# Kernel tuning notes

Hardware: AMD Instinct MI355X
Metric: run time of the kernel (lower is better)

Reference implementation:

```python
import jax, jax.numpy as jnp
import numpy as np

B, T, C, H = 4, 2048, 1024, 16
DH = C // H


def setup_inputs() -> dict:
    key = jax.random.key(0)
    k1, k2, k3 = jax.random.split(key, 3)
    x = jax.random.normal(k1, (B, T, C), dtype=jnp.float32)
    w_attn = jax.random.normal(k2, (C, 3 * C), dtype=jnp.float32) * 0.02
    w_proj = jax.random.normal(k3, (C, C), dtype=jnp.float32) * 0.02
    return {"x": x, "w_attn": w_attn, "w_proj": w_proj}


def reference(x, w_attn, w_proj):
    b, t, c = x.shape
    qkv = x @ w_attn  # [B,T,3C]
    q, k, v = jnp.split(qkv, 3, axis=2)
    # [B,T,C] -> [B,H,T,DH]
    q = q.reshape(b, t, H, DH).transpose(0, 2, 1, 3)
    k = k.reshape(b, t, H, DH).transpose(0, 2, 1, 3)
    v = v.reshape(b, t, H, DH).transpose(0, 2, 1, 3)
    scale = 1.0 / np.sqrt(DH).astype(np.float32)
    att = jnp.einsum('bhqd,bhkd->bhqk', q, k) * scale  # [B,H,T,T]
    causal = jnp.tril(jnp.ones((t, t), dtype=bool))
    att = jnp.where(causal[None, None], att, jnp.finfo(att.dtype).min)
    att = jax.nn.softmax(att, axis=-1)
    y = jnp.einsum('bhqk,bhkd->bhqd', att, v)  # [B,H,T,DH]
    y = y.transpose(0, 2, 1, 3).reshape(b, t, c)
    return y @ w_proj
```

## Files before the change

### kernel.cpp

```cpp
#include <hip/hip_runtime.h>
#include <hip/hip_bf16.h>

typedef unsigned short u16;
typedef __attribute__((ext_vector_type(8))) __bf16 bf16x8;
typedef __attribute__((ext_vector_type(4))) float f32x4;
typedef __attribute__((ext_vector_type(16))) float f32x16;
typedef u16 u16x8 __attribute__((ext_vector_type(8)));
typedef u16x8 u16x8a __attribute__((may_alias));
typedef f32x4 f32x4a __attribute__((may_alias));

constexpr int Bz = 4, T = 2048, Cdim = 1024, H = 16, DH = 64;
constexpr int Mrows = Bz * T;
constexpr int N_QKV = 3 * Cdim;
constexpr int Kdim = Cdim;
constexpr float C1 = 0.18033688011118324f;
constexpr float C2 = 34.62468098133512f;

__device__ __forceinline__ u16 f2bf(float f) {
    union { float f; unsigned u; } x; x.f = f;
    if ((x.u & 0x7f800000u) == 0x7f800000u) return 0;
    unsigned r = x.u + 0x7fffu + ((x.u >> 16) & 1u);
    return (u16)(r >> 16);
}

__device__ __forceinline__ bf16x8 as_bf(u16x8 v) {
    union { u16x8 u; bf16x8 b; } x; x.u = v; return x.b;
}

__device__ __forceinline__ void gload_lds16(const u16* g, u16* l) {
    __builtin_amdgcn_global_load_lds(
        (const __attribute__((address_space(1))) void*)g,
        (__attribute__((address_space(3))) void*)l, 16, 0, 0);
}

__device__ __forceinline__ float exp2_raw(float x) {
    float r;
    asm("v_exp_f32 %0, %1" : "=v"(r) : "v"(x));
    return r;
}

__global__ __launch_bounds__(256) void prep_kernel(
    const float* __restrict__ X, u16* __restrict__ Xb, long n8,
    const float* __restrict__ W1, u16* __restrict__ WT1,
    const float* __restrict__ W2, u16* __restrict__ WT2)
{
    const int bid = blockIdx.x;
    if (bid < 2048) {
        for (long i = bid * 256 + threadIdx.x; i < n8; i += (long)2048 * 256) {
            f32x4 a0 = *(const f32x4a*)&X[i * 8];
            f32x4 a1 = *(const f32x4a*)&X[i * 8 + 4];
            u16x8 p;
            p[0] = f2bf(a0[0]); p[1] = f2bf(a0[1]); p[2] = f2bf(a0[2]); p[3] = f2bf(a0[3]);
            p[4] = f2bf(a1[0]); p[5] = f2bf(a1[1]); p[6] = f2bf(a1[2]); p[7] = f2bf(a1[3]);
            *(u16x8a*)&Xb[i * 8] = p;
        }
    } else if (bid < 3584) {
        const int tb = bid - 2048;
        const int n = (tb % (N_QKV / 256)) * 256 + threadIdx.x;
        const int k8 = (tb / (N_QKV / 256)) * 8;
        u16x8 p;
#pragma unroll
        for (int i = 0; i < 8; ++i) p[i] = f2bf(W1[(long)(k8 + i) * N_QKV + n]);
        *(u16x8a*)&WT1[(long)n * Kdim + k8] = p;
    } else {
        const int tb = bid - 3584;
        const int n = (tb % (Cdim / 256)) * 256 + threadIdx.x;
        const int k8 = (tb / (Cdim / 256)) * 8;
        u16x8 p;
#pragma unroll
        for (int i = 0; i < 8; ++i) p[i] = f2bf(W2[(long)(k8 + i) * Cdim + n]);
        *(u16x8a*)&WT2[(long)n * Kdim + k8] = p;
    }
}

__global__ __launch_bounds__(256) void transpose_cvt(
    const float* __restrict__ W, u16* __restrict__ WT, int K, int N)
{
    const int n = blockIdx.x * 256 + threadIdx.x;
    const int k8 = blockIdx.y * 8;
    u16x8 p;
#pragma unroll
    for (int i = 0; i < 8; ++i) p[i] = f2bf(W[(long)(k8 + i) * N + n]);
    *(u16x8a*)&WT[(long)n * K + k8] = p;
}

template <int MODE>
__global__ __launch_bounds__(256) void gemm_kernel(
    const u16* __restrict__ Ab, const u16* __restrict__ Bw,
    float* __restrict__ out,
    u16* __restrict__ qb, u16* __restrict__ kb, u16* __restrict__ vtb,
    int Nsz, int Ksz)
{
    constexpr int BM = 128, BN = 128, BK = 64;
    __shared__ __align__(16) u16 As[BM * BK];
    __shared__ __align__(16) u16 Bt[BN * BK];

    const int tid = threadIdx.x;
    const int w = tid >> 6, lane = tid & 63, quad = lane >> 4, lr = lane & 15;
    const int wr = (w >> 1) * 64, wc = (w & 1) * 64;
    const int m0 = blockIdx.y * BM, n0 = blockIdx.x * BN;
    const int lr7 = lr & 7;

    const int lrow = lane >> 3;
    const int lcol = ((lane & 7) ^ lrow) * 8;

    f32x4 acc[4][4] = {};

    for (int k0 = 0; k0 < Ksz; k0 += BK) {
#pragma unroll
        for (int s = 0; s < 4; ++s) {
            const int chunk = w * 4 + s;
            const int r = chunk * 8 + lrow;
            const u16* asrc;
            if (MODE == 1) {
                asrc = &Ab[(long)(m0 + r) * Ksz + k0 + lcol];
            } else {
                const int m = m0 + r, b = m >> 11, t = m & (T - 1), h = k0 >> 6;
                asrc = &Ab[(((long)(b * H + h)) * T + t) * DH + lcol];
            }
            gload_lds16(asrc, &As[chunk * 512]);
            gload_lds16(&Bw[(long)(n0 + r) * Ksz + k0 + lcol], &Bt[chunk * 512]);
        }
        __syncthreads();

#pragma unroll
        for (int ks = 0; ks < 2; ++ks) {
            bf16x8 af[4];
#pragma unroll
            for (int it = 0; it < 4; ++it)
                af[it] = as_bf(*(const u16x8a*)
                    &As[(wr + it * 16 + lr) * BK + (((ks * 4 + quad) ^ lr7) * 8)]);
#pragma unroll
            for (int jt = 0; jt < 4; ++jt) {
                bf16x8 bfv = as_bf(*(const u16x8a*)
                    &Bt[(wc + jt * 16 + lr) * BK + (((ks * 4 + quad) ^ lr7) * 8)]);
#pragma unroll
                for (int it = 0; it < 4; ++it)
                    acc[it][jt] = __builtin_amdgcn_mfma_f32_16x16x32_bf16(af[it], bfv, acc[it][jt], 0, 0, 0);
            }
        }
        __syncthreads();
    }

#pragma unroll
    for (int it = 0; it < 4; ++it) {
#pragma unroll
        for (int jt = 0; jt < 4; ++jt) {
#pragma unroll
            for (int r = 0; r < 4; ++r) {
                int m = m0 + wr + it * 16 + quad * 4 + r;
                int n = n0 + wc + jt * 16 + lr;
                if (MODE == 2) {
                    out[(long)m * Nsz + n] = acc[it][jt][r];
                } else {
                    u16 hv = f2bf(acc[it][jt][r]);
                    int b = m >> 11, t = m & (T - 1);
                    int sec = n >> 10, rem = n & 1023, h = rem >> 6, d = rem & 63;
                    int bh = b * H + h;
                    if (sec == 0)      qb [((long)bh * T + t) * DH + d] = hv;
                    else if (sec == 1) kb [((long)bh * T + t) * DH + d] = hv;
                    else               vtb[((long)bh * DH + d) * T + t] = hv;
                }
            }
        }
    }
}

__global__ __launch_bounds__(256) void attn_kernel(
    const u16* qbuf, const u16* __restrict__ kbuf,
    const u16* __restrict__ vtbuf, u16* yb)
{
    constexpr int KS = 72;
    __shared__ __align__(16) u16 Ks[2][64 * KS];
    __shared__ __align__(16) u16 Vts[2][64 * KS];

    const int tid = threadIdx.x;
    const int w = tid >> 6, lane = tid & 63;
    const int l31 = lane & 31, hi = lane >> 5, hi4 = hi * 4, hi8 = hi * 8;
    const int bh    = blockIdx.x;
    const int pairi = blockIdx.y;

    const u16* qbase  = qbuf  + (long)bh * T * DH;
    const u16* kbase  = kbuf  + (long)bh * T * DH;
    const u16* vtbase = vtbuf + (long)bh * DH * T;
    u16* ybase = yb + (long)bh * T * DH;

    const int sr0 = tid >> 3;
    const int sc0 = (tid & 7) * 8;

    u16x8 ones_u;
#pragma unroll
    for (int i = 0; i < 8; ++i) ones_u[i] = 0x3F80;
    const bf16x8 onesf = as_bf(ones_u);

    for (int qsel = 0; qsel < 2; ++qsel) {
        const int qblk = qsel ? (15 - pairi) : pairi;
        const int q0 = qblk * 128;

        bf16x8 qf[4];
#pragma unroll
        for (int dsl = 0; dsl < 4; ++dsl)
            qf[dsl] = as_bf(*(const u16x8a*)
                &qbase[(q0 + w * 32 + l31) * DH + dsl * 16 + hi8]);

        f32x16 o[2] = {};
        f32x16 accl = {};

        const int ktmax = 2 * qblk + 1;

        u16x8 kreg[2], vreg[2];
#pragma unroll
        for (int s = 0; s < 2; ++s) {
            int row = sr0 + s * 32;
            kreg[s] = *(const u16x8a*)&kbase[(long)row * DH + sc0];
            vreg[s] = *(const u16x8a*)&vtbase[(long)row * T + sc0];
        }

        for (int kt = 0; kt <= ktmax; ++kt) {
            const int buf = kt & 1;
#pragma unroll
            for (int s = 0; s < 2; ++s) {
                int row = sr0 + s * 32;
                *(u16x8a*)&Ks[buf][row * KS + sc0]  = kreg[s];
                *(u16x8a*)&Vts[buf][row * KS + sc0] = vreg[s];
            }
            __syncthreads();

            if (kt < ktmax) {
#pragma unroll
                for (int s = 0; s < 2; ++s) {
                    int row = sr0 + s * 32;
                    kreg[s] = *(const u16x8a*)&kbase[(long)((kt + 1) * 64 + row) * DH + sc0];
                    vreg[s] = *(const u16x8a*)&vtbase[(long)row * T + (kt + 1) * 64 + sc0];
                }
            }

            f32x16 sp[2] = {};
#pragma unroll
            for (int dsl = 0; dsl < 4; ++dsl) {
#pragma unroll
                for (int nt = 0; nt < 2; ++nt) {
                    bf16x8 kf = as_bf(*(const u16x8a*)
                        &Ks[buf][(nt * 32 + l31) * KS + dsl * 16 + hi8]);
                    sp[nt] = __builtin_amdgcn_mfma_f32_32x32x16_bf16(
                        kf, qf[dsl], sp[nt], 0, 0, 0);
                }
            }

            const bool need_mask = (kt >= 2 * qblk);
            const int qrow = q0 + w * 32 + l31;
#pragma unroll
            for (int nt = 0; nt < 2; ++nt) {
#pragma unroll
                for (int reg = 0; reg < 16; ++reg) {
                    float e = exp2_raw(__builtin_fmaf(sp[nt][reg], C1, -C2));
                    if (need_mask) {
                        int key = kt * 64 + nt * 32 + ((reg & 3) + 8 * (reg >> 2)) + hi4;
                        e = (key <= qrow) ? e : 0.f;
                    }
                    sp[nt][reg] = e;
                }
            }

            unsigned wv[2][8];
#pragma unroll
            for (int nt = 0; nt < 2; ++nt)
#pragma unroll
                for (int g = 0; g < 4; ++g)
#pragma unroll
                    for (int h = 0; h < 2; ++h)
                        asm("v_cvt_pk_bf16_f32 %0, %1, %2"
                            : "=v"(wv[nt][g * 2 + h])
                            : "v"(sp[nt][g * 4 + 2 * h]), "v"(sp[nt][g * 4 + 2 * h + 1]));

#pragma unroll
            for (int sl = 0; sl < 4; ++sl) {
                const int nt = sl >> 1, s2 = (sl & 1) * 2;
                unsigned a0 = wv[nt][s2 * 2 + 0], a1 = wv[nt][s2 * 2 + 1];
                unsigned a2 = wv[nt][(s2 + 1) * 2 + 0], a3 = wv[nt][(s2 + 1) * 2 + 1];
                asm("v_permlane32_swap_b32 %0, %1" : "+v"(a0), "+v"(a2));
                asm("v_permlane32_swap_b32 %0, %1" : "+v"(a1), "+v"(a3));
                union { unsigned u[4]; bf16x8 b; } pk;
                pk.u[0] = a0; pk.u[1] = a1; pk.u[2] = a2; pk.u[3] = a3;
                accl = __builtin_amdgcn_mfma_f32_32x32x16_bf16(
                    pk.b, onesf, accl, 0, 0, 0);
#pragma unroll
                for (int dt = 0; dt < 2; ++dt) {
                    bf16x8 vf = as_bf(*(const u16x8a*)
                        &Vts[buf][(dt * 32 + l31) * KS + sl * 16 + hi8]);
                    o[dt] = __builtin_amdgcn_mfma_f32_32x32x16_bf16(
                        pk.b, vf, o[dt], 0, 0, 0);
                }
            }
        }

#pragma unroll
        for (int reg = 0; reg < 16; ++reg) {
            float rl;
            asm("v_rcp_f32 %0, %1" : "=v"(rl) : "v"(accl[reg]));
            const int cr = (reg & 3) + 8 * (reg >> 2) + hi4;
            const int t = q0 + w * 32 + cr;
#pragma unroll
            for (int dt = 0; dt < 2; ++dt)
                ybase[(long)t * DH + dt * 32 + l31] = f2bf(o[dt][reg] * rl);
        }
    }
}

extern "C" void kernel_launch(void* const* d_in, const int* in_sizes, int n_in,
                              void* d_out, int out_size, void* d_ws, size_t ws_size,
                              hipStream_t stream) {
    const float* x      = (const float*)d_in[0];
    const float* w_attn = (const float*)d_in[1];
    const float* w_proj = (const float*)d_in[2];
    float* out = (float*)d_out;

    const size_t per = (size_t)Bz * H * T * DH;
    u16* qb  = (u16*)d_ws;
    u16* kb  = qb + per;
    u16* vtb = kb + per;

    u16* xb     = (u16*)d_out;
    u16* watT   = xb + (size_t)Mrows * Kdim;

    const bool big_ws = ws_size >= ((size_t)50 << 20);
    u16* wprojT = big_ws ? (u16*)((char*)d_ws + ((size_t)48 << 20)) : kb;

    dim3 blk(256);
    prep_kernel<<<dim3(big_ws ? 4096 : 3584), blk, 0, stream>>>(
        x, xb, (long)Mrows * Kdim / 8, w_attn, watT, w_proj, wprojT);
    gemm_kernel<1><<<dim3(N_QKV / 128, Mrows / 128), blk, 0, stream>>>(
        xb, watT, nullptr, qb, kb, vtb, N_QKV, Kdim);
    attn_kernel<<<dim3(64, 8), blk, 0, stream>>>(qb, kb, vtb, qb);
    if (!big_ws)
        transpose_cvt<<<dim3(Cdim / 256, Kdim / 8), blk, 0, stream>>>(
            w_proj, wprojT, Kdim, Cdim);
    gemm_kernel<2><<<dim3(Cdim / 128, Mrows / 128), blk, 0, stream>>>(
        qb, wprojT, out, nullptr, nullptr, nullptr, Cdim, Kdim);
}
```

Before: 263.2 us.

## Process both paired query blocks in one KV sweep to share K/V tile loads

Rather than looping over the two paired query blocks one after another, the kernel now keeps both query blocks' fragments and accumulators live and walks the key/value tiles once, up to the larger block's causal limit. Each staged K/V tile in shared memory is consumed by block B and, while still within its causal range, by block A. This removes the second pass of global loads, LDS stores and barriers for the shorter block. The cost is roughly double the accumulator and query registers, which may lower occupancy or cause spills.

```diff
diff --git a/kernel.cpp b/kernel.cpp
--- a/kernel.cpp
+++ b/kernel.cpp
@@ -193,116 +193,128 @@
     for (int i = 0; i < 8; ++i) ones_u[i] = 0x3F80;
     const bf16x8 onesf = as_bf(ones_u);
 
-    for (int qsel = 0; qsel < 2; ++qsel) {
-        const int qblk = qsel ? (15 - pairi) : pairi;
-        const int q0 = qblk * 128;
-
-        bf16x8 qf[4];
-#pragma unroll
-        for (int dsl = 0; dsl < 4; ++dsl)
-            qf[dsl] = as_bf(*(const u16x8a*)
-                &qbase[(q0 + w * 32 + l31) * DH + dsl * 16 + hi8]);
-
-        f32x16 o[2] = {};
-        f32x16 accl = {};
-
-        const int ktmax = 2 * qblk + 1;
-
-        u16x8 kreg[2], vreg[2];
+    const int qbA = pairi, qbB = 15 - pairi;
+    const int q0A = qbA * 128, q0B = qbB * 128;
+    const int ktmaxA = 2 * qbA + 1;
+    const int ktmaxB = 2 * qbB + 1;
+
+    bf16x8 qfA[4], qfB[4];
+#pragma unroll
+    for (int dsl = 0; dsl < 4; ++dsl) {
+        qfA[dsl] = as_bf(*(const u16x8a*)
+            &qbase[(q0A + w * 32 + l31) * DH + dsl * 16 + hi8]);
+        qfB[dsl] = as_bf(*(const u16x8a*)
+            &qbase[(q0B + w * 32 + l31) * DH + dsl * 16 + hi8]);
+    }
+
+    f32x16 oA[2] = {}, oB[2] = {};
+    f32x16 acclA = {}, acclB = {};
+
+    auto compute = [&](const bf16x8* qf, f32x16* o, f32x16& accl,
+                       int q0, int qblk, int kt, int buf) {
+        f32x16 sp[2] = {};
+#pragma unroll
+        for (int dsl = 0; dsl < 4; ++dsl) {
+#pragma unroll
+            for (int nt = 0; nt < 2; ++nt) {
+                bf16x8 kf = as_bf(*(const u16x8a*)
+                    &Ks[buf][(nt * 32 + l31) * KS + dsl * 16 + hi8]);
+                sp[nt] = __builtin_amdgcn_mfma_f32_32x32x16_bf16(
+                    kf, qf[dsl], sp[nt], 0, 0, 0);
+            }
+        }
+
+        const bool need_mask = (kt >= 2 * qblk);
+        const int qrow = q0 + w * 32 + l31;
+#pragma unroll
+        for (int nt = 0; nt < 2; ++nt) {
+#pragma unroll
+            for (int reg = 0; reg < 16; ++reg) {
+                float e = exp2_raw(__builtin_fmaf(sp[nt][reg], C1, -C2));
+                if (need_mask) {
+                    int key = kt * 64 + nt * 32 + ((reg & 3) + 8 * (reg >> 2)) + hi4;
+                    e = (key <= qrow) ? e : 0.f;
+                }
+                sp[nt][reg] = e;
+            }
+        }
+
+        unsigned wv[2][8];
+#pragma unroll
+        for (int nt = 0; nt < 2; ++nt)
+#pragma unroll
+            for (int g = 0; g < 4; ++g)
+#pragma unroll
+                for (int h = 0; h < 2; ++h)
+                    asm("v_cvt_pk_bf16_f32 %0, %1, %2"
+                        : "=v"(wv[nt][g * 2 + h])
+                        : "v"(sp[nt][g * 4 + 2 * h]), "v"(sp[nt][g * 4 + 2 * h + 1]));
+
+#pragma unroll
+        for (int sl = 0; sl < 4; ++sl) {
+            const int nt = sl >> 1, s2 = (sl & 1) * 2;
+            unsigned a0 = wv[nt][s2 * 2 + 0], a1 = wv[nt][s2 * 2 + 1];
+            unsigned a2 = wv[nt][(s2 + 1) * 2 + 0], a3 = wv[nt][(s2 + 1) * 2 + 1];
+            asm("v_permlane32_swap_b32 %0, %1" : "+v"(a0), "+v"(a2));
+            asm("v_permlane32_swap_b32 %0, %1" : "+v"(a1), "+v"(a3));
+            union { unsigned u[4]; bf16x8 b; } pk;
+            pk.u[0] = a0; pk.u[1] = a1; pk.u[2] = a2; pk.u[3] = a3;
+            accl = __builtin_amdgcn_mfma_f32_32x32x16_bf16(
+                pk.b, onesf, accl, 0, 0, 0);
+#pragma unroll
+            for (int dt = 0; dt < 2; ++dt) {
+                bf16x8 vf = as_bf(*(const u16x8a*)
+                    &Vts[buf][(dt * 32 + l31) * KS + sl * 16 + hi8]);
+                o[dt] = __builtin_amdgcn_mfma_f32_32x32x16_bf16(
+                    pk.b, vf, o[dt], 0, 0, 0);
+            }
+        }
+    };
+
+    u16x8 kreg[2], vreg[2];
+#pragma unroll
+    for (int s = 0; s < 2; ++s) {
+        int row = sr0 + s * 32;
+        kreg[s] = *(const u16x8a*)&kbase[(long)row * DH + sc0];
+        vreg[s] = *(const u16x8a*)&vtbase[(long)row * T + sc0];
+    }
+
+    for (int kt = 0; kt <= ktmaxB; ++kt) {
+        const int buf = kt & 1;
 #pragma unroll
         for (int s = 0; s < 2; ++s) {
             int row = sr0 + s * 32;
-            kreg[s] = *(const u16x8a*)&kbase[(long)row * DH + sc0];
-            vreg[s] = *(const u16x8a*)&vtbase[(long)row * T + sc0];
-        }
-
-        for (int kt = 0; kt <= ktmax; ++kt) {
-            const int buf = kt & 1;
+            *(u16x8a*)&Ks[buf][row * KS + sc0]  = kreg[s];
+            *(u16x8a*)&Vts[buf][row * KS + sc0] = vreg[s];
+        }
+        __syncthreads();
+
+        if (kt < ktmaxB) {
 #pragma unroll
             for (int s = 0; s < 2; ++s) {
                 int row = sr0 + s * 32;
-                *(u16x8a*)&Ks[buf][row * KS + sc0]  = kreg[s];
-                *(u16x8a*)&Vts[buf][row * KS + sc0] = vreg[s];
-            }
-            __syncthreads();
-
-            if (kt < ktmax) {
-#pragma unroll
-                for (int s = 0; s < 2; ++s) {
-                    int row = sr0 + s * 32;
-                    kreg[s] = *(const u16x8a*)&kbase[(long)((kt + 1) * 64 + row) * DH + sc0];
-                    vreg[s] = *(const u16x8a*)&vtbase[(long)row * T + (kt + 1) * 64 + sc0];
-                }
-            }
-
-            f32x16 sp[2] = {};
-#pragma unroll
-            for (int dsl = 0; dsl < 4; ++dsl) {
-#pragma unroll
-                for (int nt = 0; nt < 2; ++nt) {
-                    bf16x8 kf = as_bf(*(const u16x8a*)
-                        &Ks[buf][(nt * 32 + l31) * KS + dsl * 16 + hi8]);
-                    sp[nt] = __builtin_amdgcn_mfma_f32_32x32x16_bf16(
-                        kf, qf[dsl], sp[nt], 0, 0, 0);
-                }
-            }
-
-            const bool need_mask = (kt >= 2 * qblk);
-            const int qrow = q0 + w * 32 + l31;
-#pragma unroll
-            for (int nt = 0; nt < 2; ++nt) {
-#pragma unroll
-                for (int reg = 0; reg < 16; ++reg) {
-                    float e = exp2_raw(__builtin_fmaf(sp[nt][reg], C1, -C2));
-                    if (need_mask) {
-                        int key = kt * 64 + nt * 32 + ((reg & 3) + 8 * (reg >> 2)) + hi4;
-                        e = (key <= qrow) ? e : 0.f;
-                    }
-                    sp[nt][reg] = e;
-                }
-            }
-
-            unsigned wv[2][8];
-#pragma unroll
-            for (int nt = 0; nt < 2; ++nt)
-#pragma unroll
-                for (int g = 0; g < 4; ++g)
-#pragma unroll
-                    for (int h = 0; h < 2; ++h)
-                        asm("v_cvt_pk_bf16_f32 %0, %1, %2"
-                            : "=v"(wv[nt][g * 2 + h])
-                            : "v"(sp[nt][g * 4 + 2 * h]), "v"(sp[nt][g * 4 + 2 * h + 1]));
-
-#pragma unroll
-            for (int sl = 0; sl < 4; ++sl) {
-                const int nt = sl >> 1, s2 = (sl & 1) * 2;
-                unsigned a0 = wv[nt][s2 * 2 + 0], a1 = wv[nt][s2 * 2 + 1];
-                unsigned a2 = wv[nt][(s2 + 1) * 2 + 0], a3 = wv[nt][(s2 + 1) * 2 + 1];
-                asm("v_permlane32_swap_b32 %0, %1" : "+v"(a0), "+v"(a2));
-                asm("v_permlane32_swap_b32 %0, %1" : "+v"(a1), "+v"(a3));
-                union { unsigned u[4]; bf16x8 b; } pk;
-                pk.u[0] = a0; pk.u[1] = a1; pk.u[2] = a2; pk.u[3] = a3;
-                accl = __builtin_amdgcn_mfma_f32_32x32x16_bf16(
-                    pk.b, onesf, accl, 0, 0, 0);
-#pragma unroll
-                for (int dt = 0; dt < 2; ++dt) {
-                    bf16x8 vf = as_bf(*(const u16x8a*)
-                        &Vts[buf][(dt * 32 + l31) * KS + sl * 16 + hi8]);
-                    o[dt] = __builtin_amdgcn_mfma_f32_32x32x16_bf16(
-                        pk.b, vf, o[dt], 0, 0, 0);
-                }
-            }
-        }
-
-#pragma unroll
-        for (int reg = 0; reg < 16; ++reg) {
-            float rl;
-            asm("v_rcp_f32 %0, %1" : "=v"(rl) : "v"(accl[reg]));
-            const int cr = (reg & 3) + 8 * (reg >> 2) + hi4;
-            const int t = q0 + w * 32 + cr;
-#pragma unroll
-            for (int dt = 0; dt < 2; ++dt)
-                ybase[(long)t * DH + dt * 32 + l31] = f2bf(o[dt][reg] * rl);
+                kreg[s] = *(const u16x8a*)&kbase[(long)((kt + 1) * 64 + row) * DH + sc0];
+                vreg[s] = *(const u16x8a*)&vtbase[(long)row * T + (kt + 1) * 64 + sc0];
+            }
+        }
+
+        compute(qfB, oB, acclB, q0B, qbB, kt, buf);
+        if (kt <= ktmaxA)
+            compute(qfA, oA, acclA, q0A, qbA, kt, buf);
+    }
+
+#pragma unroll
+    for (int reg = 0; reg < 16; ++reg) {
+        float rlA, rlB;
+        asm("v_rcp_f32 %0, %1" : "=v"(rlA) : "v"(acclA[reg]));
+        asm("v_rcp_f32 %0, %1" : "=v"(rlB) : "v"(acclB[reg]));
+        const int cr = (reg & 3) + 8 * (reg >> 2) + hi4;
+        const int tA = q0A + w * 32 + cr;
+        const int tB = q0B + w * 32 + cr;
+#pragma unroll
+        for (int dt = 0; dt < 2; ++dt) {
+            ybase[(long)tA * DH + dt * 32 + l31] = f2bf(oA[dt][reg] * rlA);
+            ybase[(long)tB * DH + dt * 32 + l31] = f2bf(oB[dt][reg] * rlB);
         }
     }
 }
```

New measurement: 292.7 us. 11.2% more time.
